# Performance work log

Measured on AMD Instinct MI355X. Metric: run time of the kernel, lower is better.

## Reference

```python
import jax, jax.numpy as jnp
import numpy as np

H = 32        # query heads
KVH = 8       # kv heads
HD = 64       # head_dim
N_REP = H // KVH
THETA = 10000.0


def _rope_cos_sin(seq_len, dim):
    # freqs_cis[t, i] = exp(1j * t * theta^{-2i/dim}) -> return cos, sin [S, dim//2]
    inv_freq = 1.0 / (THETA ** (jnp.arange(0, dim, 2, dtype=jnp.float32) / dim))
    t = jnp.arange(seq_len, dtype=jnp.float32)
    freqs = jnp.outer(t, inv_freq)  # [S, dim//2]
    return jnp.cos(freqs), jnp.sin(freqs)


def _apply_rope(x, cos, sin):
    # x: [B, S, h, HD]; pairs are interleaved (even=real, odd=imag)
    xr = x[..., 0::2]
    xi = x[..., 1::2]
    c = cos[None, :, None, :]
    s = sin[None, :, None, :]
    out_r = xr * c - xi * s
    out_i = xr * s + xi * c
    return jnp.stack([out_r, out_i], axis=-1).reshape(x.shape)


def setup_inputs() -> dict:
    key = jax.random.key(0)
    ks = jax.random.split(key, 5)
    D = 2048
    B, S = 1, 2048
    scale = 0.02
    return {
        "hidden_states": jax.random.normal(ks[0], (B, S, D), jnp.float32),
        "Wq": jax.random.normal(ks[1], (D, H * HD), jnp.float32) * scale,
        "Wk": jax.random.normal(ks[2], (D, KVH * HD), jnp.float32) * scale,
        "Wv": jax.random.normal(ks[3], (D, KVH * HD), jnp.float32) * scale,
        "Wo": jax.random.normal(ks[4], (H * HD, D), jnp.float32) * scale,
    }


def reference(hidden_states, Wq, Wk, Wv, Wo):
    B, S, D = hidden_states.shape
    xq = (hidden_states @ Wq).reshape(B, S, H, HD)
    xk = (hidden_states @ Wk).reshape(B, S, KVH, HD)
    xv = (hidden_states @ Wv).reshape(B, S, KVH, HD)

    cos, sin = _rope_cos_sin(S, HD)
    xq = _apply_rope(xq, cos, sin)
    xk = _apply_rope(xk, cos, sin)

    # GQA: expand kv heads (kv head g -> query heads g*N_REP .. g*N_REP+N_REP-1)
    keys = jnp.repeat(xk, N_REP, axis=2)    # [B, S, H, HD]
    values = jnp.repeat(xv, N_REP, axis=2)

    q = xq.transpose(0, 2, 1, 3)      # [B, H, S, HD]
    k = keys.transpose(0, 2, 1, 3)
    v = values.transpose(0, 2, 1, 3)

    scores = jnp.einsum('bhqd,bhkd->bhqk', q, k) / jnp.sqrt(jnp.float32(HD))
    causal = jnp.tril(jnp.ones((S, S), dtype=bool))
    scores = jnp.where(causal[None, None], scores, jnp.float32(-jnp.inf))
    probs = jax.nn.softmax(scores.astype(jnp.float32), axis=-1).astype(q.dtype)

    out = jnp.einsum('bhqk,bhkd->bhqd', probs, v)   # [B, H, S, HD]
    out = out.transpose(0, 2, 1, 3).reshape(B, S, H * HD)
    return out @ Wo
```

## Files before the change

### kernel.cpp

```cpp
#include <hip/hip_runtime.h>


#define NH  32
#define NKV 8

typedef __attribute__((ext_vector_type(8))) __bf16 bf16x8;
typedef __attribute__((ext_vector_type(4))) __bf16 bf16x4;
typedef __attribute__((ext_vector_type(4))) float  f32x4;

#define SCALE_LOG2 0.18033688011112042f
#define L2_10K_32  0.41524101186098665f

__device__ __forceinline__ void glds16(const __bf16* g, __bf16* l) {
  __builtin_amdgcn_global_load_lds(
      (const __attribute__((address_space(1))) unsigned int*)g,
      (__attribute__((address_space(3))) unsigned int*)l, 16, 0, 0);
}

__device__ __forceinline__ float pair_swap(float v) {
  int t = __builtin_amdgcn_mov_dpp(__builtin_bit_cast(int, v), 0xB1, 0xf, 0xf, true);
  return __builtin_bit_cast(float, t);
}

__device__ __forceinline__ unsigned pack_bf16(float lo, float hi) {
  union { __bf16 b[2]; unsigned u; } r;
  r.b[0] = (__bf16)lo; r.b[1] = (__bf16)hi;
  return r.u;
}

__global__ __launch_bounds__(256) void k_prep(
    const float* __restrict__ hx, const float* __restrict__ Wq,
    const float* __restrict__ Wk, const float* __restrict__ Wv,
    const float* __restrict__ Wo, __bf16* __restrict__ Xb,
    __bf16* __restrict__ Wqkvt, __bf16* __restrict__ Wot) {
  __shared__ float t[32 * 36];
  const int nt = blockIdx.x, k0 = blockIdx.y * 32;
  const int tid = threadIdx.x;
  const int r = tid >> 3, c4 = (tid & 7) * 4;
  if (nt >= 160) {
    int c0 = (nt - 160) * 32;
    float4 v = *(const float4*)(hx + (size_t)(k0 + r) * 2048 + c0 + c4);
    bf16x4 o;
    o[0] = (__bf16)v.x; o[1] = (__bf16)v.y; o[2] = (__bf16)v.z; o[3] = (__bf16)v.w;
    *(bf16x4*)(Xb + (size_t)(k0 + r) * 2048 + c0 + c4) = o;
    return;
  }
  const float* W; int ldW, n0; __bf16* dst;
  if (nt < 64)      { W = Wq; ldW = 2048; dst = Wqkvt;                       n0 = nt * 32; }
  else if (nt < 80) { W = Wk; ldW = 512;  dst = Wqkvt + (size_t)2048 * 2048; n0 = (nt - 64) * 32; }
  else if (nt < 96) { W = Wv; ldW = 512;  dst = Wqkvt + (size_t)2560 * 2048; n0 = (nt - 80) * 32; }
  else              { W = Wo; ldW = 2048; dst = Wot;                         n0 = (nt - 96) * 32; }
  float4 v = *(const float4*)(W + (size_t)(k0 + r) * ldW + n0 + c4);
  *(float4*)(t + r * 36 + ((((c4 >> 2) ^ r) & 7) << 2)) = v;
  __syncthreads();
  bf16x4 o;
#pragma unroll
  for (int j = 0; j < 4; j++) {
    int kk = c4 + j;
    o[j] = (__bf16)t[kk * 36 + ((((r >> 2) ^ kk) & 7) << 2) + (r & 3)];
  }
  *(bf16x4*)(dst + (size_t)(n0 + r) * 2048 + k0 + c4) = o;
}

__global__ void k_vtrans_b(const __bf16* __restrict__ V, __bf16* __restrict__ Vt) {
  __shared__ __bf16 t[32][33];
  int c0 = blockIdx.x * 32, s0 = blockIdx.y * 32;
  int tx = threadIdx.x, ty = threadIdx.y;
#pragma unroll
  for (int j = 0; j < 4; j++)
    t[ty + j * 8][tx] = V[(size_t)(s0 + ty + j * 8) * 512 + c0 + tx];
  __syncthreads();
#pragma unroll
  for (int j = 0; j < 4; j++)
    Vt[(size_t)(c0 + ty + j * 8) * 2048 + s0 + tx] = t[tx][ty + j * 8];
}

__global__ __launch_bounds__(256) void k_gemm_qkv(
    const __bf16* __restrict__ A, const __bf16* __restrict__ Bt,
    __bf16* __restrict__ Qb, __bf16* __restrict__ Kb, __bf16* __restrict__ Vb) {
  const int K = 2048;
  __shared__ __bf16 As[64][32];
  __shared__ __bf16 Bs[128][32];
  const int tid = threadIdx.x;
  const int m0 = blockIdx.x * 64, n0 = blockIdx.y * 128;
  const int w = tid >> 6, lane = tid & 63, quad = lane >> 4, lid = lane & 15;
  const int wm = (w & 1) * 32, wn = (w >> 1) * 64;
  const int r0 = tid >> 2;
  const int cg = (((tid & 3) ^ ((tid >> 3) & 3)) * 8);
  const __bf16* Ag = A + (size_t)(m0 + r0) * K + cg;
  const __bf16* Bg = Bt + (size_t)(n0 + r0) * K + cg;
  __bf16* Asl = &As[0][0] + tid * 8;
  __bf16* Bsl = &Bs[0][0] + tid * 8;
  const int csw = ((quad ^ ((lid >> 1) & 3)) * 8);
  f32x4 acc[2][4] = {};
  for (int k0 = 0; k0 < K; k0 += 32) {
    __syncthreads();
    glds16(Ag + k0, Asl);
    glds16(Bg + k0, Bsl);
    glds16(Bg + (size_t)64 * K + k0, Bsl + 2048);
    __syncthreads();
    bf16x8 a[2], b[4];
#pragma unroll
    for (int mt = 0; mt < 2; mt++)
      a[mt] = *(const bf16x8*)(&As[wm + mt * 16 + lid][csw]);
#pragma unroll
    for (int nt = 0; nt < 4; nt++)
      b[nt] = *(const bf16x8*)(&Bs[wn + nt * 16 + lid][csw]);
#pragma unroll
    for (int mt = 0; mt < 2; mt++)
#pragma unroll
      for (int nt = 0; nt < 4; nt++)
        acc[mt][nt] = __builtin_amdgcn_mfma_f32_16x16x32_bf16(
            a[mt], b[nt], acc[mt][nt], 0, 0, 0);
  }
  if (n0 >= 2560) {
#pragma unroll
    for (int mt = 0; mt < 2; mt++)
#pragma unroll
      for (int nt = 0; nt < 4; nt++)
#pragma unroll
        for (int i = 0; i < 4; i++) {
          int mm = m0 + wm + mt * 16 + quad * 4 + i;
          int nn = n0 + wn + nt * 16 + lid - 2560;
          Vb[(size_t)mm * 512 + nn] = (__bf16)acc[mt][nt][i];
        }
  } else {
    const bool isQ = (n0 < 2048);
    const float scale = isQ ? SCALE_LOG2 : 1.0f;
    __bf16* dst = isQ ? Qb : Kb;
    const int ldd = isQ ? 2048 : 512;
    const int noff = isQ ? 0 : 2048;
    const bool odd = lid & 1;
#pragma unroll
    for (int nt = 0; nt < 4; nt++) {
      int nn = n0 + wn + nt * 16 + lid;
      int fi = (nn & 63) >> 1;
      float inv = __builtin_amdgcn_exp2f(-(float)fi * L2_10K_32);
#pragma unroll
      for (int mt = 0; mt < 2; mt++)
#pragma unroll
        for (int i = 0; i < 4; i++) {
          int mm = m0 + wm + mt * 16 + quad * 4 + i;
          float ang = (float)mm * inv;
          float sn, cs;
          __sincosf(ang, &sn, &cs);
          float v = acc[mt][nt][i];
          float p = __shfl_xor(v, 1);
          float o = v * cs + (odd ? p : -p) * sn;
          dst[(size_t)mm * ldd + nn - noff] = (__bf16)(o * scale);
        }
    }
  }
}

__global__ __launch_bounds__(256) void k_gemm_out(
    const __bf16* __restrict__ A, const __bf16* __restrict__ Bt,
    float* __restrict__ C) {
  const int K = 2048, N = 2048;
  __shared__ __bf16 As[64][32];
  __shared__ __bf16 Bs[128][32];
  const int tid = threadIdx.x;
  const int m0 = blockIdx.x * 64, n0 = blockIdx.y * 128;
  const int w = tid >> 6, lane = tid & 63, quad = lane >> 4, lid = lane & 15;
  const int wm = (w & 1) * 32, wn = (w >> 1) * 64;
  const int r0 = tid >> 2;
  const int cg = (((tid & 3) ^ ((tid >> 3) & 3)) * 8);
  const __bf16* Ag = A + (size_t)(m0 + r0) * K + cg;
  const __bf16* Bg = Bt + (size_t)(n0 + r0) * K + cg;
  __bf16* Asl = &As[0][0] + tid * 8;
  __bf16* Bsl = &Bs[0][0] + tid * 8;
  const int csw = ((quad ^ ((lid >> 1) & 3)) * 8);
  f32x4 acc[2][4] = {};
  for (int k0 = 0; k0 < K; k0 += 32) {
    __syncthreads();
    glds16(Ag + k0, Asl);
    glds16(Bg + k0, Bsl);
    glds16(Bg + (size_t)64 * K + k0, Bsl + 2048);
    __syncthreads();
    bf16x8 a[2], b[4];
#pragma unroll
    for (int mt = 0; mt < 2; mt++)
      a[mt] = *(const bf16x8*)(&As[wm + mt * 16 + lid][csw]);
#pragma unroll
    for (int nt = 0; nt < 4; nt++)
      b[nt] = *(const bf16x8*)(&Bs[wn + nt * 16 + lid][csw]);
#pragma unroll
    for (int mt = 0; mt < 2; mt++)
#pragma unroll
      for (int nt = 0; nt < 4; nt++)
        acc[mt][nt] = __builtin_amdgcn_mfma_f32_16x16x32_bf16(
            a[mt], b[nt], acc[mt][nt], 0, 0, 0);
  }
#pragma unroll
  for (int mt = 0; mt < 2; mt++)
#pragma unroll
    for (int nt = 0; nt < 4; nt++)
#pragma unroll
      for (int i = 0; i < 4; i++) {
        int mm = m0 + wm + mt * 16 + quad * 4 + i;
        int nn = n0 + wn + nt * 16 + lid;
        C[(size_t)mm * N + nn] = acc[mt][nt][i];
      }
}

__global__ __launch_bounds__(256, 4) void k_attn(
    const __bf16* __restrict__ Q, const __bf16* __restrict__ Kc,
    const __bf16* __restrict__ Vt, __bf16* __restrict__ Oc) {
  __shared__ char smem[26624];
  __bf16* KsB = (__bf16*)smem;
  __bf16* VsB = (__bf16*)(smem + 8192);
  __bf16* PsB = (__bf16*)(smem + 16384);
  float*  OL  = (float*)smem;
  float*  Lsh = (float*)(smem + 17408);
  const int h = blockIdx.x;
  const int qt = 31 - blockIdx.y;
  const int q0 = qt * 64;
  const int kvh = h >> 2;
  const int tid = threadIdx.x;
  const int w = tid >> 6, lane = tid & 63, quad = lane >> 4, lid = lane & 15;
  const int qh = w & 1, kh = w >> 1;
  const int r0 = tid >> 3;
  const int cg0 = (((tid & 7) ^ (r0 & 7)) * 8);

  bf16x8 aq[2][2];
#pragma unroll
  for (int mt = 0; mt < 2; mt++)
#pragma unroll
    for (int ks = 0; ks < 2; ks++)
      aq[mt][ks] = *(const bf16x8*)(
          Q + (size_t)(q0 + qh * 32 + mt * 16 + lid) * 2048 + h * 64 +
          ks * 32 + quad * 8);

  bf16x8 bone;
#pragma unroll
  for (int j = 0; j < 8; j++) bone[j] = (lid == 0) ? (__bf16)1.0f : (__bf16)0.0f;

  const __bf16* Kg = Kc + kvh * 64 + cg0;
  const __bf16* Vg = Vt + ((size_t)(kvh * 64 + r0)) * 2048 + cg0;
  __bf16* Pw = PsB + w * 1280;

  f32x4 Oacc[2][4] = {};
  f32x4 Lacc[2] = {};

  for (int kt = 0; kt <= qt; kt++) {
    const int kv0 = kt * 64;
    glds16(Kg + (size_t)(kv0 + r0) * 512,        KsB + tid * 8);
    glds16(Kg + (size_t)(kv0 + r0 + 32) * 512,   KsB + (tid + 256) * 8);
    glds16(Vg + kv0,                             VsB + tid * 8);
    glds16(Vg + (size_t)32 * 2048 + kv0,         VsB + (tid + 256) * 8);
    __syncthreads();

    f32x4 Sc[2][2] = {};
#pragma unroll
    for (int nt = 0; nt < 2; nt++) {
      int krow = kh * 32 + nt * 16 + lid;
      int cl = (quad ^ (lid & 7)) * 8;
      bf16x8 b0 = *(const bf16x8*)(KsB + krow * 64 + cl);
      bf16x8 b1 = *(const bf16x8*)(KsB + krow * 64 + (cl ^ 32));
#pragma unroll
      for (int mt = 0; mt < 2; mt++) {
        Sc[mt][nt] = __builtin_amdgcn_mfma_f32_16x16x32_bf16(aq[mt][0], b0, Sc[mt][nt], 0, 0, 0);
        Sc[mt][nt] = __builtin_amdgcn_mfma_f32_16x16x32_bf16(aq[mt][1], b1, Sc[mt][nt], 0, 0, 0);
      }
    }
    if (kt == qt) {
#pragma unroll
      for (int mt = 0; mt < 2; mt++)
#pragma unroll
        for (int nt = 0; nt < 2; nt++)
#pragma unroll
          for (int i = 0; i < 4; i++) {
            int kvg = kv0 + kh * 32 + nt * 16 + lid;
            int qrg = q0 + qh * 32 + mt * 16 + quad * 4 + i;
            if (kvg > qrg) Sc[mt][nt][i] = -1e30f;
          }
    }

#pragma unroll
    for (int mt = 0; mt < 2; mt++)
#pragma unroll
      for (int i = 0; i < 4; i++) {
        float pA = __builtin_amdgcn_exp2f(Sc[mt][0][i]);
        float pB = __builtin_amdgcn_exp2f(Sc[mt][1][i]);
        float send = (lid & 1) ? pA : pB;
        float recv = pair_swap(send);
        float lo = (lid & 1) ? recv : pA;
        float hi = (lid & 1) ? pB : recv;
        int row = mt * 16 + quad * 4 + i;
        int col = (lid & 1) ? (lid + 15) : lid;
        *(unsigned*)(Pw + row * 40 + col) = pack_bf16(lo, hi);
      }

    bf16x8 ap[2];
#pragma unroll
    for (int mt = 0; mt < 2; mt++)
      ap[mt] = *(const bf16x8*)(Pw + (mt * 16 + lid) * 40 + quad * 8);
#pragma unroll
    for (int mt = 0; mt < 2; mt++)
      Lacc[mt] = __builtin_amdgcn_mfma_f32_16x16x32_bf16(ap[mt], bone, Lacc[mt], 0, 0, 0);
#pragma unroll
    for (int nt = 0; nt < 4; nt++) {
      bf16x8 bv = *(const bf16x8*)(
          VsB + (nt * 16 + lid) * 64 + (((kh * 4 + quad) ^ (lid & 7)) * 8));
#pragma unroll
      for (int mt = 0; mt < 2; mt++)
        Oacc[mt][nt] = __builtin_amdgcn_mfma_f32_16x16x32_bf16(ap[mt], bv, Oacc[mt][nt], 0, 0, 0);
    }
    __syncthreads();
  }

  if (kh == 1) {
#pragma unroll
    for (int mt = 0; mt < 2; mt++)
#pragma unroll
      for (int nt = 0; nt < 4; nt++)
#pragma unroll
        for (int i = 0; i < 4; i++)
          OL[qh * 2176 + (mt * 16 + quad * 4 + i) * 68 + nt * 16 + lid] =
              Oacc[mt][nt][i];
    if (lid == 0)
#pragma unroll
      for (int mt = 0; mt < 2; mt++)
#pragma unroll
        for (int i = 0; i < 4; i++)
          Lsh[qh * 32 + mt * 16 + quad * 4 + i] = Lacc[mt][i];
  }
  __syncthreads();
  if (kh == 0) {
#pragma unroll
    for (int mt = 0; mt < 2; mt++)
#pragma unroll
      for (int i = 0; i < 4; i++) {
        int row = mt * 16 + quad * 4 + i;
        float lsum = __shfl(Lacc[mt][i], lane & 48) + Lsh[qh * 32 + row];
        float rs = 1.0f / lsum;
#pragma unroll
        for (int nt = 0; nt < 4; nt++) {
          float o = Oacc[mt][nt][i] + OL[qh * 2176 + row * 68 + nt * 16 + lid];
          Oc[(size_t)(q0 + qh * 32 + row) * 2048 + h * 64 + nt * 16 + lid] =
              (__bf16)(o * rs);
        }
      }
  }
}

extern "C" void kernel_launch(void* const* d_in, const int* in_sizes, int n_in,
                              void* d_out, int out_size, void* d_ws, size_t ws_size,
                              hipStream_t stream) {
  const float* hx = (const float*)d_in[0];
  const float* Wq = (const float*)d_in[1];
  const float* Wk = (const float*)d_in[2];
  const float* Wv = (const float*)d_in[3];
  const float* Wo = (const float*)d_in[4];
  float* out = (float*)d_out;

  char* ws = (char*)d_ws;
  size_t off = 0;
  auto alloc = [&](size_t bytes) -> void* {
    void* p = ws + off;
    off += (bytes + 255) & ~(size_t)255;
    return p;
  };
  __bf16* Xb    = (__bf16*)alloc((size_t)2048 * 2048 * 2);
  __bf16* Wqkvt = (__bf16*)alloc((size_t)3072 * 2048 * 2);
  __bf16* Wot   = (__bf16*)alloc((size_t)2048 * 2048 * 2);
  __bf16* Qb    = (__bf16*)alloc((size_t)2048 * 2048 * 2);
  __bf16* Kb    = (__bf16*)alloc((size_t)2048 * 512 * 2);
  __bf16* Vb    = (__bf16*)alloc((size_t)2048 * 512 * 2);
  __bf16* Vtg   = (__bf16*)alloc((size_t)512 * 2048 * 2);
  __bf16* AOb   = (__bf16*)alloc((size_t)2048 * 2048 * 2);

  k_prep<<<dim3(224, 64), 256, 0, stream>>>(hx, Wq, Wk, Wv, Wo, Xb, Wqkvt, Wot);
  k_gemm_qkv<<<dim3(32, 24), 256, 0, stream>>>(Xb, Wqkvt, Qb, Kb, Vb);
  k_vtrans_b<<<dim3(16, 64), dim3(32, 8), 0, stream>>>(Vb, Vtg);
  k_attn<<<dim3(NH, 32), 256, 0, stream>>>(Qb, Kb, Vtg, AOb);
  k_gemm_out<<<dim3(32, 16), 256, 0, stream>>>(AOb, Wot, out);
}
```

Baseline: 216.4 us.

## Widen GEMM K-tile to 64 and load attention K/V fragments directly from global

```diff
diff --git a/kernel.cpp b/kernel.cpp
--- a/kernel.cpp
+++ b/kernel.cpp
@@ -79,39 +79,49 @@
     const __bf16* __restrict__ A, const __bf16* __restrict__ Bt,
     __bf16* __restrict__ Qb, __bf16* __restrict__ Kb, __bf16* __restrict__ Vb) {
   const int K = 2048;
-  __shared__ __bf16 As[64][32];
-  __shared__ __bf16 Bs[128][32];
+  __shared__ __bf16 As[64][64];
+  __shared__ __bf16 Bs[128][64];
   const int tid = threadIdx.x;
   const int m0 = blockIdx.x * 64, n0 = blockIdx.y * 128;
   const int w = tid >> 6, lane = tid & 63, quad = lane >> 4, lid = lane & 15;
   const int wm = (w & 1) * 32, wn = (w >> 1) * 64;
-  const int r0 = tid >> 2;
-  const int cg = (((tid & 3) ^ ((tid >> 3) & 3)) * 8);
-  const __bf16* Ag = A + (size_t)(m0 + r0) * K + cg;
-  const __bf16* Bg = Bt + (size_t)(n0 + r0) * K + cg;
+  const int r0 = tid >> 3;
+  const int cg0 = (((tid & 7) ^ (r0 & 7)) * 8);
+  const __bf16* Ag = A + (size_t)(m0 + r0) * K + cg0;
+  const __bf16* Bg = Bt + (size_t)(n0 + r0) * K + cg0;
   __bf16* Asl = &As[0][0] + tid * 8;
   __bf16* Bsl = &Bs[0][0] + tid * 8;
-  const int csw = ((quad ^ ((lid >> 1) & 3)) * 8);
+  const int cl = ((quad ^ (lid & 7)) * 8);
   f32x4 acc[2][4] = {};
-  for (int k0 = 0; k0 < K; k0 += 32) {
+  for (int k0 = 0; k0 < K; k0 += 64) {
     __syncthreads();
     glds16(Ag + k0, Asl);
+    glds16(Ag + (size_t)32 * K + k0, Asl + 2048);
     glds16(Bg + k0, Bsl);
-    glds16(Bg + (size_t)64 * K + k0, Bsl + 2048);
+    glds16(Bg + (size_t)32 * K + k0, Bsl + 2048);
+    glds16(Bg + (size_t)64 * K + k0, Bsl + 4096);
+    glds16(Bg + (size_t)96 * K + k0, Bsl + 6144);
     __syncthreads();
-    bf16x8 a[2], b[4];
-#pragma unroll
-    for (int mt = 0; mt < 2; mt++)
-      a[mt] = *(const bf16x8*)(&As[wm + mt * 16 + lid][csw]);
-#pragma unroll
-    for (int nt = 0; nt < 4; nt++)
-      b[nt] = *(const bf16x8*)(&Bs[wn + nt * 16 + lid][csw]);
-#pragma unroll
-    for (int mt = 0; mt < 2; mt++)
-#pragma unroll
-      for (int nt = 0; nt < 4; nt++)
+    bf16x8 a[2][2], b[4][2];
+#pragma unroll
+    for (int mt = 0; mt < 2; mt++) {
+      a[mt][0] = *(const bf16x8*)(&As[wm + mt * 16 + lid][cl]);
+      a[mt][1] = *(const bf16x8*)(&As[wm + mt * 16 + lid][cl ^ 32]);
+    }
+#pragma unroll
+    for (int nt = 0; nt < 4; nt++) {
+      b[nt][0] = *(const bf16x8*)(&Bs[wn + nt * 16 + lid][cl]);
+      b[nt][1] = *(const bf16x8*)(&Bs[wn + nt * 16 + lid][cl ^ 32]);
+    }
+#pragma unroll
+    for (int mt = 0; mt < 2; mt++)
+#pragma unroll
+      for (int nt = 0; nt < 4; nt++) {
         acc[mt][nt] = __builtin_amdgcn_mfma_f32_16x16x32_bf16(
-            a[mt], b[nt], acc[mt][nt], 0, 0, 0);
+            a[mt][0], b[nt][0], acc[mt][nt], 0, 0, 0);
+        acc[mt][nt] = __builtin_amdgcn_mfma_f32_16x16x32_bf16(
+            a[mt][1], b[nt][1], acc[mt][nt], 0, 0, 0);
+      }
   }
   if (n0 >= 2560) {
 #pragma unroll
@@ -157,39 +167,49 @@
     const __bf16* __restrict__ A, const __bf16* __restrict__ Bt,
     float* __restrict__ C) {
   const int K = 2048, N = 2048;
-  __shared__ __bf16 As[64][32];
-  __shared__ __bf16 Bs[128][32];
+  __shared__ __bf16 As[64][64];
+  __shared__ __bf16 Bs[128][64];
   const int tid = threadIdx.x;
   const int m0 = blockIdx.x * 64, n0 = blockIdx.y * 128;
   const int w = tid >> 6, lane = tid & 63, quad = lane >> 4, lid = lane & 15;
   const int wm = (w & 1) * 32, wn = (w >> 1) * 64;
-  const int r0 = tid >> 2;
-  const int cg = (((tid & 3) ^ ((tid >> 3) & 3)) * 8);
-  const __bf16* Ag = A + (size_t)(m0 + r0) * K + cg;
-  const __bf16* Bg = Bt + (size_t)(n0 + r0) * K + cg;
+  const int r0 = tid >> 3;
+  const int cg0 = (((tid & 7) ^ (r0 & 7)) * 8);
+  const __bf16* Ag = A + (size_t)(m0 + r0) * K + cg0;
+  const __bf16* Bg = Bt + (size_t)(n0 + r0) * K + cg0;
   __bf16* Asl = &As[0][0] + tid * 8;
   __bf16* Bsl = &Bs[0][0] + tid * 8;
-  const int csw = ((quad ^ ((lid >> 1) & 3)) * 8);
+  const int cl = ((quad ^ (lid & 7)) * 8);
   f32x4 acc[2][4] = {};
-  for (int k0 = 0; k0 < K; k0 += 32) {
+  for (int k0 = 0; k0 < K; k0 += 64) {
     __syncthreads();
     glds16(Ag + k0, Asl);
+    glds16(Ag + (size_t)32 * K + k0, Asl + 2048);
     glds16(Bg + k0, Bsl);
-    glds16(Bg + (size_t)64 * K + k0, Bsl + 2048);
+    glds16(Bg + (size_t)32 * K + k0, Bsl + 2048);
+    glds16(Bg + (size_t)64 * K + k0, Bsl + 4096);
+    glds16(Bg + (size_t)96 * K + k0, Bsl + 6144);
     __syncthreads();
-    bf16x8 a[2], b[4];
-#pragma unroll
-    for (int mt = 0; mt < 2; mt++)
-      a[mt] = *(const bf16x8*)(&As[wm + mt * 16 + lid][csw]);
-#pragma unroll
-    for (int nt = 0; nt < 4; nt++)
-      b[nt] = *(const bf16x8*)(&Bs[wn + nt * 16 + lid][csw]);
-#pragma unroll
-    for (int mt = 0; mt < 2; mt++)
-#pragma unroll
-      for (int nt = 0; nt < 4; nt++)
+    bf16x8 a[2][2], b[4][2];
+#pragma unroll
+    for (int mt = 0; mt < 2; mt++) {
+      a[mt][0] = *(const bf16x8*)(&As[wm + mt * 16 + lid][cl]);
+      a[mt][1] = *(const bf16x8*)(&As[wm + mt * 16 + lid][cl ^ 32]);
+    }
+#pragma unroll
+    for (int nt = 0; nt < 4; nt++) {
+      b[nt][0] = *(const bf16x8*)(&Bs[wn + nt * 16 + lid][cl]);
+      b[nt][1] = *(const bf16x8*)(&Bs[wn + nt * 16 + lid][cl ^ 32]);
+    }
+#pragma unroll
+    for (int mt = 0; mt < 2; mt++)
+#pragma unroll
+      for (int nt = 0; nt < 4; nt++) {
         acc[mt][nt] = __builtin_amdgcn_mfma_f32_16x16x32_bf16(
-            a[mt], b[nt], acc[mt][nt], 0, 0, 0);
+            a[mt][0], b[nt][0], acc[mt][nt], 0, 0, 0);
+        acc[mt][nt] = __builtin_amdgcn_mfma_f32_16x16x32_bf16(
+            a[mt][1], b[nt][1], acc[mt][nt], 0, 0, 0);
+      }
   }
 #pragma unroll
   for (int mt = 0; mt < 2; mt++)
@@ -206,12 +226,9 @@
 __global__ __launch_bounds__(256, 4) void k_attn(
     const __bf16* __restrict__ Q, const __bf16* __restrict__ Kc,
     const __bf16* __restrict__ Vt, __bf16* __restrict__ Oc) {
-  __shared__ char smem[26624];
-  __bf16* KsB = (__bf16*)smem;
-  __bf16* VsB = (__bf16*)(smem + 8192);
-  __bf16* PsB = (__bf16*)(smem + 16384);
-  float*  OL  = (float*)smem;
-  float*  Lsh = (float*)(smem + 17408);
+  __shared__ __bf16 Ps[4][32][40];
+  __shared__ float OL[2][32][68];
+  __shared__ float Lsh[64];
   const int h = blockIdx.x;
   const int qt = 31 - blockIdx.y;
   const int q0 = qt * 64;
@@ -219,8 +236,6 @@
   const int tid = threadIdx.x;
   const int w = tid >> 6, lane = tid & 63, quad = lane >> 4, lid = lane & 15;
   const int qh = w & 1, kh = w >> 1;
-  const int r0 = tid >> 3;
-  const int cg0 = (((tid & 7) ^ (r0 & 7)) * 8);
 
   bf16x8 aq[2][2];
 #pragma unroll
@@ -235,34 +250,35 @@
 #pragma unroll
   for (int j = 0; j < 8; j++) bone[j] = (lid == 0) ? (__bf16)1.0f : (__bf16)0.0f;
 
-  const __bf16* Kg = Kc + kvh * 64 + cg0;
-  const __bf16* Vg = Vt + ((size_t)(kvh * 64 + r0)) * 2048 + cg0;
-  __bf16* Pw = PsB + w * 1280;
+  const __bf16* Kfr = Kc + (size_t)(kh * 32 + lid) * 512 + kvh * 64 + quad * 8;
+  const __bf16* Vfr = Vt + (size_t)(kvh * 64 + lid) * 2048 + kh * 32 + quad * 8;
 
   f32x4 Oacc[2][4] = {};
   f32x4 Lacc[2] = {};
 
   for (int kt = 0; kt <= qt; kt++) {
     const int kv0 = kt * 64;
-    glds16(Kg + (size_t)(kv0 + r0) * 512,        KsB + tid * 8);
-    glds16(Kg + (size_t)(kv0 + r0 + 32) * 512,   KsB + (tid + 256) * 8);
-    glds16(Vg + kv0,                             VsB + tid * 8);
-    glds16(Vg + (size_t)32 * 2048 + kv0,         VsB + (tid + 256) * 8);
-    __syncthreads();
+    bf16x8 kf[2][2];
+#pragma unroll
+    for (int nt = 0; nt < 2; nt++)
+#pragma unroll
+      for (int ch = 0; ch < 2; ch++)
+        kf[nt][ch] = *(const bf16x8*)(Kfr + (size_t)(kv0 + nt * 16) * 512 + ch * 32);
+    bf16x8 vf[4];
+#pragma unroll
+    for (int nt = 0; nt < 4; nt++)
+      vf[nt] = *(const bf16x8*)(Vfr + (size_t)nt * 16 * 2048 + kv0);
 
     f32x4 Sc[2][2] = {};
 #pragma unroll
-    for (int nt = 0; nt < 2; nt++) {
-      int krow = kh * 32 + nt * 16 + lid;
-      int cl = (quad ^ (lid & 7)) * 8;
-      bf16x8 b0 = *(const bf16x8*)(KsB + krow * 64 + cl);
-      bf16x8 b1 = *(const bf16x8*)(KsB + krow * 64 + (cl ^ 32));
+    for (int nt = 0; nt < 2; nt++)
 #pragma unroll
       for (int mt = 0; mt < 2; mt++) {
-        Sc[mt][nt] = __builtin_amdgcn_mfma_f32_16x16x32_bf16(aq[mt][0], b0, Sc[mt][nt], 0, 0, 0);
-        Sc[mt][nt] = __builtin_amdgcn_mfma_f32_16x16x32_bf16(aq[mt][1], b1, Sc[mt][nt], 0, 0, 0);
-      }
-    }
+        Sc[mt][nt] = __builtin_amdgcn_mfma_f32_16x16x32_bf16(
+            aq[mt][0], kf[nt][0], Sc[mt][nt], 0, 0, 0);
+        Sc[mt][nt] = __builtin_amdgcn_mfma_f32_16x16x32_bf16(
+            aq[mt][1], kf[nt][1], Sc[mt][nt], 0, 0, 0);
+      }
     if (kt == qt) {
 #pragma unroll
       for (int mt = 0; mt < 2; mt++)
@@ -288,25 +304,22 @@
         float hi = (lid & 1) ? pB : recv;
         int row = mt * 16 + quad * 4 + i;
         int col = (lid & 1) ? (lid + 15) : lid;
-        *(unsigned*)(Pw + row * 40 + col) = pack_bf16(lo, hi);
+        *(unsigned*)(&Ps[w][row][col]) = pack_bf16(lo, hi);
       }
 
     bf16x8 ap[2];
 #pragma unroll
     for (int mt = 0; mt < 2; mt++)
-      ap[mt] = *(const bf16x8*)(Pw + (mt * 16 + lid) * 40 + quad * 8);
+      ap[mt] = *(const bf16x8*)(&Ps[w][mt * 16 + lid][quad * 8]);
 #pragma unroll
     for (int mt = 0; mt < 2; mt++)
       Lacc[mt] = __builtin_amdgcn_mfma_f32_16x16x32_bf16(ap[mt], bone, Lacc[mt], 0, 0, 0);
 #pragma unroll
-    for (int nt = 0; nt < 4; nt++) {
-      bf16x8 bv = *(const bf16x8*)(
-          VsB + (nt * 16 + lid) * 64 + (((kh * 4 + quad) ^ (lid & 7)) * 8));
+    for (int nt = 0; nt < 4; nt++)
 #pragma unroll
       for (int mt = 0; mt < 2; mt++)
-        Oacc[mt][nt] = __builtin_amdgcn_mfma_f32_16x16x32_bf16(ap[mt], bv, Oacc[mt][nt], 0, 0, 0);
-    }
-    __syncthreads();
+        Oacc[mt][nt] = __builtin_amdgcn_mfma_f32_16x16x32_bf16(
+            ap[mt], vf[nt], Oacc[mt][nt], 0, 0, 0);
   }
 
   if (kh == 1) {
@@ -316,8 +329,7 @@
       for (int nt = 0; nt < 4; nt++)
 #pragma unroll
         for (int i = 0; i < 4; i++)
-          OL[qh * 2176 + (mt * 16 + quad * 4 + i) * 68 + nt * 16 + lid] =
-              Oacc[mt][nt][i];
+          OL[qh][mt * 16 + quad * 4 + i][nt * 16 + lid] = Oacc[mt][nt][i];
     if (lid == 0)
 #pragma unroll
       for (int mt = 0; mt < 2; mt++)
@@ -336,7 +348,7 @@
         float rs = 1.0f / lsum;
 #pragma unroll
         for (int nt = 0; nt < 4; nt++) {
-          float o = Oacc[mt][nt][i] + OL[qh * 2176 + row * 68 + nt * 16 + lid];
+          float o = Oacc[mt][nt][i] + OL[qh][row][nt * 16 + lid];
           Oc[(size_t)(q0 + qh * 32 + row) * 2048 + h * 64 + nt * 16 + lid] =
               (__bf16)(o * rs);
         }
```

After: 239.5 us. 10.6% more time.
